# Performance work log

Measured on AMD Instinct MI355X. Metric: run time of the kernel, lower is better.

Reference implementation:

```python
import jax, jax.numpy as jnp
import numpy as np
from jax import lax

DN = ('NCHW', 'OIHW', 'NCHW')

def conv2d(x, w, b, stride, pad):
    y = lax.conv_general_dilated(x, w, (stride, stride), [(pad, pad), (pad, pad)], dimension_numbers=DN)
    return y + b[None, :, None, None]

def conv_transpose2d(x, w, b):
    # torch ConvTranspose2d(k=4, s=2, p=1): weight is (in, out, kH, kW).
    # Equivalent dilated conv: flip spatial dims, swap in/out, lhs_dilation=2, pad=k-1-p=2.
    kernel = jnp.flip(w, (2, 3)).transpose(1, 0, 2, 3)  # (out, in, 4, 4)
    y = lax.conv_general_dilated(x, kernel, (1, 1), [(2, 2), (2, 2)], lhs_dilation=(2, 2), dimension_numbers=DN)
    return y + b[None, :, None, None]

def res_block(x, w, b):
    return x + jax.nn.relu(conv2d(x, w, b, 1, 1))

def setup_inputs() -> dict:
    key = jax.random.key(0)
    ks = jax.random.split(key, 20)
    F_, K, D = 16, 64, 16  # num_features, num_embeddings, embedding_dim
    s = 0.05
    inp = {
        'x': jax.random.normal(ks[0], (64, 1, 256, 256), jnp.float32),
        'conv1_w': jax.random.normal(ks[1], (F_, 1, 4, 4), jnp.float32) * s,
        'conv1_b': jnp.zeros((F_,), jnp.float32),
        'conv2_w': jax.random.normal(ks[2], (F_, F_, 4, 4), jnp.float32) * s,
        'conv2_b': jnp.zeros((F_,), jnp.float32),
        'er1_w': jax.random.normal(ks[3], (F_, F_, 3, 3), jnp.float32) * s,
        'er1_b': jnp.zeros((F_,), jnp.float32),
        'er2_w': jax.random.normal(ks[4], (F_, F_, 3, 3), jnp.float32) * s,
        'er2_b': jnp.zeros((F_,), jnp.float32),
        'codebook': jax.random.normal(ks[5], (K, D), jnp.float32),
        'dr1_w': jax.random.normal(ks[6], (F_, F_, 3, 3), jnp.float32) * s,
        'dr1_b': jnp.zeros((F_,), jnp.float32),
        'dr2_w': jax.random.normal(ks[7], (F_, F_, 3, 3), jnp.float32) * s,
        'dr2_b': jnp.zeros((F_,), jnp.float32),
        'tc1_w': jax.random.normal(ks[8], (F_, F_, 4, 4), jnp.float32) * s,  # ConvTranspose (in,out,kH,kW)
        'tc1_b': jnp.zeros((F_,), jnp.float32),
        'tc2_w': jax.random.normal(ks[9], (F_, 1, 4, 4), jnp.float32) * s,
        'tc2_b': jnp.zeros((1,), jnp.float32),
    }
    return inp

def reference(x, conv1_w, conv1_b, conv2_w, conv2_b, er1_w, er1_b, er2_w, er2_b,
              codebook, dr1_w, dr1_b, dr2_w, dr2_b, tc1_w, tc1_b, tc2_w, tc2_b):
    # Encoder
    h = jax.nn.relu(conv2d(x, conv1_w, conv1_b, 2, 1))
    h = jax.nn.relu(conv2d(h, conv2_w, conv2_b, 2, 1))
    h = res_block(h, er1_w, er1_b)
    h = res_block(h, er2_w, er2_b)  # (B, 16, 64, 64)
    # VQ: faithful to torch's encoded.view(-1, C) raw NCHW flatten
    C = h.shape[1]
    flat = h.reshape(-1, C)  # (N, 16)
    # squared L2 distances without materializing (N, K, D) broadcast tensor
    d = (jnp.sum(flat * flat, axis=1, keepdims=True)
         - 2.0 * flat @ codebook.T
         + jnp.sum(codebook * codebook, axis=1)[None, :])  # (N, K)
    indices = jnp.argmin(d, axis=1)  # (N,)
    quantized = codebook[indices].reshape(h.shape)
    # Decoder
    q = res_block(quantized, dr1_w, dr1_b)
    q = res_block(q, dr2_w, dr2_b)
    q = jax.nn.relu(conv_transpose2d(q, tc1_w, tc1_b))
    decoded = conv_transpose2d(q, tc2_w, tc2_b)  # (B, 1, 256, 256)
    return decoded, indices
```

## Files before the change

kernel.cpp:

```cpp
#include <hip/hip_runtime.h>
#include <hip/hip_bf16.h>


#define R8X(M)  M(0) M(1) M(2) M(3) M(4) M(5) M(6) M(7)

typedef __attribute__((ext_vector_type(8))) short          bf16x8;
typedef __attribute__((ext_vector_type(8))) unsigned short u16x8;
typedef __attribute__((ext_vector_type(4))) float          f32x4;

__device__ __forceinline__ unsigned short f2bf(float f) {
    unsigned u; __builtin_memcpy(&u, &f, 4);
    unsigned r = u + 0x7FFFu + ((u >> 16) & 1u);
    return (unsigned short)(r >> 16);
}
__device__ __forceinline__ float bf2f(unsigned short h) {
    unsigned u = ((unsigned)h) << 16;
    float f; __builtin_memcpy(&f, &u, 4);
    return f;
}

__global__ __launch_bounds__(256) void conv1_k(const float* __restrict__ x, const float* __restrict__ w,
                                               const float* __restrict__ bias,
                                               unsigned short* __restrict__ oh, unsigned short* __restrict__ ol) {
    int idx = blockIdx.x * 256 + threadIdx.x;
    int ox = idx & 127;
    int oy = (idx >> 7) & 127;
    int b  = idx >> 14;
    const float* xin = x + (size_t)b * 65536;
    float pv[16];
#pragma unroll
    for (int ky = 0; ky < 4; ++ky) {
        int iy = 2 * oy - 1 + ky;
#pragma unroll
        for (int kx = 0; kx < 4; ++kx) {
            int ix = 2 * ox - 1 + kx;
            pv[ky * 4 + kx] = (iy >= 0 && iy < 256 && ix >= 0 && ix < 256)
                                  ? xin[iy * 256 + ix] : 0.f;
        }
    }
    u16x8 h0, h1, l0, l1;
#pragma unroll
    for (int oc = 0; oc < 16; ++oc) {
        float acc = bias[oc];
#pragma unroll
        for (int k = 0; k < 16; ++k) acc = fmaf(pv[k], w[oc * 16 + k], acc);
        float r = fmaxf(acc, 0.f);
        unsigned short hb = f2bf(r);
        unsigned short lb = f2bf(r - bf2f(hb));
        if (oc < 8) { h0[oc] = hb; l0[oc] = lb; }
        else        { h1[oc - 8] = hb; l1[oc - 8] = lb; }
    }
    u16x8* po = (u16x8*)(oh + (size_t)idx * 16);
    po[0] = h0; po[1] = h1;
    u16x8* pl = (u16x8*)(ol + (size_t)idx * 16);
    pl[0] = l0; pl[1] = l1;
}

__global__ __launch_bounds__(256) void conv2_mfma_k(const unsigned short* __restrict__ fh,
                                                    const unsigned short* __restrict__ fl,
                                                    const float* __restrict__ w, const float* __restrict__ bias,
                                                    unsigned short* __restrict__ oh, unsigned short* __restrict__ ol) {
    __shared__ unsigned short wsh[16 * 264];
    __shared__ unsigned short wsl[16 * 264];
    for (int i = threadIdx.x; i < 4096; i += 256) {
        int oc = i >> 8, k = i & 255;
        int ic = k & 15, tap = k >> 4;
        float f = w[oc * 256 + ic * 16 + tap];
        unsigned short hb = f2bf(f);
        wsh[oc * 264 + k] = hb;
        wsl[oc * 264 + k] = f2bf(f - bf2f(hb));
    }
    __syncthreads();

    int wid  = threadIdx.x >> 6;
    int lane = threadIdx.x & 63;
    int col = lane & 15;
    int kg  = lane >> 4;
    int ic0 = (kg & 1) * 8;
    float accb = bias[col];
    int gw = blockIdx.x * 4 + wid;

    for (int t = 0; t < 2; ++t) {
        int tile = gw * 2 + t;
        int v0  = (tile & 3) * 16;
        int y   = (tile >> 2) & 63;
        int img = tile >> 8;
        const unsigned short* bh = fh + (size_t)img * 262144;
        const unsigned short* bl = fl + (size_t)img * 262144;
        f32x4 acc = { accb, accb, accb, accb };
#pragma unroll
        for (int m = 0; m < 8; ++m) {
            int tap = 2 * m + (kg >> 1);
            int ty = tap >> 2, tx = tap & 3;
            int jy = 2 * y - 1 + ty;
            int jx = 2 * (v0 + col) - 1 + tx;
            bf16x8 ah = { 0, 0, 0, 0, 0, 0, 0, 0 };
            bf16x8 al = { 0, 0, 0, 0, 0, 0, 0, 0 };
            if (jy >= 0 && jy < 128 && jx >= 0 && jx < 128) {
                size_t off = ((size_t)(jy * 128 + jx)) * 16 + ic0;
                ah = *(const bf16x8*)(bh + off);
                al = *(const bf16x8*)(bl + off);
            }
            bf16x8 wh = *(const bf16x8*)&wsh[col * 264 + m * 32 + kg * 8];
            bf16x8 wl = *(const bf16x8*)&wsl[col * 264 + m * 32 + kg * 8];
            acc = __builtin_amdgcn_mfma_f32_16x16x32_bf16(ah, wh, acc, 0, 0, 0);
            acc = __builtin_amdgcn_mfma_f32_16x16x32_bf16(al, wh, acc, 0, 0, 0);
            acc = __builtin_amdgcn_mfma_f32_16x16x32_bf16(ah, wl, acc, 0, 0, 0);
        }
#pragma unroll
        for (int r = 0; r < 4; ++r) {
            int xx = v0 + kg * 4 + r;
            size_t ad = (size_t)img * 65536 + ((size_t)(y * 64 + xx)) * 16 + col;
            float rv = fmaxf(acc[r], 0.f);
            unsigned short hb = f2bf(rv);
            oh[ad] = hb;
            ol[ad] = f2bf(rv - bf2f(hb));
        }
    }
}

template <int OUTMODE>
__global__ __launch_bounds__(256) void er_mfma_k(const unsigned short* __restrict__ inh,
                                                 const unsigned short* __restrict__ inl,
                                                 const float* __restrict__ w, const float* __restrict__ bias,
                                                 unsigned short* __restrict__ oh, unsigned short* __restrict__ ol,
                                                 float* __restrict__ ofp) {
    __shared__ unsigned short wsh[16 * 176];
    __shared__ unsigned short wsl[16 * 176];
    for (int i = threadIdx.x; i < 2816; i += 256) {
        int oc = i / 176, k = i % 176;
        float f = (k < 144) ? w[(oc * 16 + (k & 15)) * 9 + (k >> 4)] : 0.f;
        unsigned short hb = f2bf(f);
        wsh[i] = hb;
        wsl[i] = f2bf(f - bf2f(hb));
    }
    __syncthreads();

    int wid  = threadIdx.x >> 6;
    int lane = threadIdx.x & 63;
    int col = lane & 15;
    int kg  = lane >> 4;
    int ic0 = (kg & 1) * 8;
    float accb = bias[col];
    int gw = blockIdx.x * 4 + wid;

    for (int t = 0; t < 8; ++t) {
        int tile = gw * 8 + t;
        int v0  = (tile & 3) * 16;
        int y   = (tile >> 2) & 63;
        int img = tile >> 8;
        const unsigned short* xh = inh + (size_t)img * 65536;
        const unsigned short* xl = inl + (size_t)img * 65536;
        f32x4 acc = { accb, accb, accb, accb };
#pragma unroll
        for (int m = 0; m < 5; ++m) {
            int tap = 2 * m + (kg >> 1);
            bf16x8 ah = { 0, 0, 0, 0, 0, 0, 0, 0 };
            bf16x8 al = { 0, 0, 0, 0, 0, 0, 0, 0 };
            if (tap < 9) {
                int ty = tap / 3, tx = tap - ty * 3;
                int jy = y + ty - 1;
                int jx = v0 + col + tx - 1;
                if (jy >= 0 && jy < 64 && jx >= 0 && jx < 64) {
                    size_t off = ((size_t)(jy * 64 + jx)) * 16 + ic0;
                    ah = *(const bf16x8*)(xh + off);
                    al = *(const bf16x8*)(xl + off);
                }
            }
            bf16x8 wh = *(const bf16x8*)&wsh[col * 176 + m * 32 + kg * 8];
            bf16x8 wl = *(const bf16x8*)&wsl[col * 176 + m * 32 + kg * 8];
            acc = __builtin_amdgcn_mfma_f32_16x16x32_bf16(ah, wh, acc, 0, 0, 0);
            acc = __builtin_amdgcn_mfma_f32_16x16x32_bf16(al, wh, acc, 0, 0, 0);
            acc = __builtin_amdgcn_mfma_f32_16x16x32_bf16(ah, wl, acc, 0, 0, 0);
        }
#pragma unroll
        for (int r = 0; r < 4; ++r) {
            int px = v0 + kg * 4 + r;
            size_t ad = ((size_t)(y * 64 + px)) * 16 + col;
            float vin = bf2f(xh[ad]) + bf2f(xl[ad]);
            float res = vin + fmaxf(acc[r], 0.f);
            if (OUTMODE == 0) {
                unsigned short hb = f2bf(res);
                oh[(size_t)img * 65536 + ad] = hb;
                ol[(size_t)img * 65536 + ad] = f2bf(res - bf2f(hb));
            } else {
                ofp[(size_t)img * 65536 + (size_t)col * 4096 + y * 64 + px] = res;
            }
        }
    }
}

__global__ __launch_bounds__(256) void vq_k(const float* __restrict__ h, const float* __restrict__ cb,
                                            unsigned short* __restrict__ q, float* __restrict__ idx_out) {
    __shared__ float cbs[1024];
    __shared__ float cn[64];
    for (int i = threadIdx.x; i < 1024; i += 256) cbs[i] = cb[i];
    __syncthreads();
    if (threadIdx.x < 64) {
        float s = 0.f;
#pragma unroll
        for (int d = 0; d < 16; ++d) { float v = cbs[threadIdx.x * 16 + d]; s = fmaf(v, v, s); }
        cn[threadIdx.x] = s;
    }
    __syncthreads();
    int r = blockIdx.x * 256 + threadIdx.x;
    float f[16];
    const float4* hp = (const float4*)(h + (size_t)r * 16);
#pragma unroll
    for (int j = 0; j < 4; ++j) {
        float4 v = hp[j];
        f[j * 4 + 0] = v.x; f[j * 4 + 1] = v.y; f[j * 4 + 2] = v.z; f[j * 4 + 3] = v.w;
    }
    float best = 3.4e38f;
    int bi = 0;
    for (int k = 0; k < 64; ++k) {
        float dot = 0.f;
#pragma unroll
        for (int d = 0; d < 16; ++d) dot = fmaf(f[d], cbs[k * 16 + d], dot);
        float dist = cn[k] - 2.f * dot;
        if (dist < best) { best = dist; bi = k; }
    }
    u16x8 q0, q1;
#pragma unroll
    for (int d = 0; d < 8; ++d) {
        q0[d] = f2bf(cbs[bi * 16 + d]);
        q1[d] = f2bf(cbs[bi * 16 + 8 + d]);
    }
    u16x8* qp = (u16x8*)(q + (size_t)r * 16);
    qp[0] = q0; qp[1] = q1;
    idx_out[r] = (float)bi;
}

__global__ __launch_bounds__(256) void trans_k(const unsigned short* __restrict__ in,
                                               unsigned short* __restrict__ out) {
    __shared__ unsigned short lds[16 * 64];
    int b = blockIdx.x >> 6;
    int y = blockIdx.x & 63;
    int t = threadIdx.x;
    {
        int c = t >> 4, x0 = (t & 15) * 4;
        const unsigned short* p = in + (((size_t)(b * 16 + c) * 64 + y) << 6) + x0;
#pragma unroll
        for (int j = 0; j < 4; ++j) lds[c * 64 + x0 + j] = p[j];
    }
    __syncthreads();
    {
        int xx = t >> 2, c0 = (t & 3) * 4;
        unsigned short* p = out + (((size_t)(b * 64 + y) * 64 + xx) << 4) + c0;
#pragma unroll
        for (int j = 0; j < 4; ++j) p[j] = lds[(c0 + j) * 64 + xx];
    }
}

__global__ __launch_bounds__(256) void res_mfma_k(const unsigned short* __restrict__ in,
                                                  const float* __restrict__ w, const float* __restrict__ bias,
                                                  unsigned short* __restrict__ outb) {
    int wid  = threadIdx.x >> 6;
    int lane = threadIdx.x & 63;
    int col = lane & 15;
    int kg  = lane >> 4;
    int ic0 = (kg & 1) * 8;

    bf16x8 bw[5];
#pragma unroll
    for (int m = 0; m < 5; ++m) {
        int tap = 2 * m + (kg >> 1);
        bf16x8 t = { 0, 0, 0, 0, 0, 0, 0, 0 };
        if (tap < 9) {
#pragma unroll
            for (int j = 0; j < 8; ++j)
                t[j] = (short)f2bf(w[(col * 16 + ic0 + j) * 9 + tap]);
        }
        bw[m] = t;
    }
    float accb = bias[col];

    int gw = blockIdx.x * 4 + wid;
    for (int t = 0; t < 8; ++t) {
        int tile = gw * 8 + t;
        int v0  = (tile & 3) * 16;
        int y   = (tile >> 2) & 63;
        int img = tile >> 8;
        const unsigned short* xi = in + (size_t)img * 65536;
        f32x4 acc = { accb, accb, accb, accb };
#pragma unroll
        for (int m = 0; m < 5; ++m) {
            int tap = 2 * m + (kg >> 1);
            bf16x8 a = { 0, 0, 0, 0, 0, 0, 0, 0 };
            if (tap < 9) {
                int ty = tap / 3, tx = tap - ty * 3;
                int jy = y + ty - 1;
                int jx = v0 + col + tx - 1;
                if (jy >= 0 && jy < 64 && jx >= 0 && jx < 64)
                    a = *(const bf16x8*)(xi + ((jy * 64 + jx) * 16 + ic0));
            }
            acc = __builtin_amdgcn_mfma_f32_16x16x32_bf16(a, bw[m], acc, 0, 0, 0);
        }
#pragma unroll
        for (int r = 0; r < 4; ++r) {
            int px = v0 + kg * 4 + r;
            size_t ad = (size_t)(y * 64 + px) * 16 + col;
            float vin = bf2f(xi[ad]);
            outb[(size_t)img * 65536 + ad] = f2bf(vin + fmaxf(acc[r], 0.f));
        }
    }
}

__global__ __launch_bounds__(256) void tconv1_mfma_k(const unsigned short* __restrict__ xb,
                                                     const float* __restrict__ w1, const float* __restrict__ bia,
                                                     unsigned short* __restrict__ outb) {
    int cls = blockIdx.x >> 9;
    int bb  = blockIdx.x & 511;
    int DY = cls >> 1, DX = cls & 1;
    int wid  = threadIdx.x >> 6;
    int lane = threadIdx.x & 63;
    int oc = lane & 15;
    int kg = lane >> 4;

    bf16x8 bfr0, bfr1;
    float accb = bia[oc];
#pragma unroll
    for (int m = 0; m < 2; ++m) {
        int tap = 2 * m + (kg >> 1);
        int ty = tap >> 1, tx = tap & 1;
        int koff = (3 - DY - 2 * ty) * 4 + (3 - DX - 2 * tx);
        int ic0 = (kg & 1) * 8;
        bf16x8 t;
#pragma unroll
        for (int j = 0; j < 8; ++j)
            t[j] = (short)f2bf(w1[(ic0 + j) * 256 + oc * 16 + koff]);
        if (m == 0) bfr0 = t; else bfr1 = t;
    }

    int Wc = bb * 4 + wid;
    for (int t = 0; t < 8; ++t) {
        int tile = Wc * 8 + t;
        int v0  = (tile & 3) * 16;
        int u   = (tile >> 2) & 63;
        int img = tile >> 8;
        const unsigned short* xi = xb + (size_t)img * 65536;
        f32x4 acc = { accb, accb, accb, accb };
#pragma unroll
        for (int m = 0; m < 2; ++m) {
            int tap = 2 * m + (kg >> 1);
            int ty = tap >> 1, tx = tap & 1;
            int jy = u + DY - 1 + ty;
            int jx = v0 + oc + DX - 1 + tx;
            bf16x8 a = { 0, 0, 0, 0, 0, 0, 0, 0 };
            if (jy >= 0 && jy < 64 && jx >= 0 && jx < 64) {
                int ic0 = (kg & 1) * 8;
                a = *(const bf16x8*)(xi + ((jy * 64 + jx) * 16 + ic0));
            }
            acc = __builtin_amdgcn_mfma_f32_16x16x32_bf16(a, (m == 0 ? bfr0 : bfr1), acc, 0, 0, 0);
        }
        int my = 2 * u + DY;
#pragma unroll
        for (int r = 0; r < 4; ++r) {
            int pxr = kg * 4 + r;
            int mx  = 2 * (v0 + pxr) + DX;
            outb[(((size_t)img * 16384) + my * 128 + mx) * 16 + oc] = f2bf(fmaxf(acc[r], 0.f));
        }
    }
}

template <int RY, int RX>
__device__ __forceinline__ void quad_contrib(const unsigned short* __restrict__ px,
                                             const float* __restrict__ w2,
                                             float& a00, float& a01, float& a10, float& a11) {
    constexpr int nY = (RY == 0) ? 2 : 1;
    constexpr int nX = (RX == 0) ? 2 : 1;
    constexpr int dyA[2] = { (RY == 1) ? 1 : 0, 1 };
    constexpr int kyA[2] = { (RY == -1) ? 3 : ((RY == 0) ? 1 : 0), 2 };
    constexpr int dxA[2] = { (RX == 1) ? 1 : 0, 1 };
    constexpr int kxA[2] = { (RX == -1) ? 3 : ((RX == 0) ? 1 : 0), 2 };
    u16x8 h0 = *(const u16x8*)px;
    u16x8 h1 = *(const u16x8*)(px + 8);
#pragma unroll
    for (int iy = 0; iy < nY; ++iy) {
#pragma unroll
        for (int ix = 0; ix < nX; ++ix) {
            const int ky = kyA[iy], kx = kxA[ix];
            float& a = (dyA[iy] == 0) ? ((dxA[ix] == 0) ? a00 : a01)
                                      : ((dxA[ix] == 0) ? a10 : a11);
#pragma unroll
            for (int ic = 0; ic < 8; ++ic)
                a = fmaf(bf2f(h0[ic]), w2[ic * 16 + ky * 4 + kx], a);
#pragma unroll
            for (int ic = 0; ic < 8; ++ic)
                a = fmaf(bf2f(h1[ic]), w2[(ic + 8) * 16 + ky * 4 + kx], a);
        }
    }
}

__global__ __launch_bounds__(256) void tconv2_quad_k(const unsigned short* __restrict__ f1b,
                                                     const float* __restrict__ w2, const float* __restrict__ b2,
                                                     float* __restrict__ out) {
    int idx = blockIdx.x * 256 + threadIdx.x;
    int v = idx & 127;
    int u = (idx >> 7) & 127;
    int b = idx >> 14;
    const unsigned short* fb = f1b + (size_t)b * 262144;
    float b2s = b2[0];
    float a00 = b2s, a01 = b2s, a10 = b2s, a11 = b2s;

#define QC(RY, RX) { int jy = u + (RY), jx = v + (RX); \
    if (jy >= 0 && jy < 128 && jx >= 0 && jx < 128) \
        quad_contrib<RY, RX>(fb + ((size_t)(jy * 128 + jx) << 4), w2, a00, a01, a10, a11); }
    QC(-1, -1) QC(-1, 0) QC(-1, 1)
    QC( 0, -1) QC( 0, 0) QC( 0, 1)
    QC( 1, -1) QC( 1, 0) QC( 1, 1)
#undef QC

    float* o = out + (size_t)b * 65536 + (2 * u) * 256 + 2 * v;
    float2 r0; r0.x = a00; r0.y = a01;
    float2 r1; r1.x = a10; r1.y = a11;
    *(float2*)o         = r0;
    *(float2*)(o + 256) = r1;
}

extern "C" void kernel_launch(void* const* d_in, const int* in_sizes, int n_in,
                              void* d_out, int out_size, void* d_ws, size_t ws_size,
                              hipStream_t stream) {
    const float* x    = (const float*)d_in[0];
    const float* c1w  = (const float*)d_in[1];
    const float* c1b  = (const float*)d_in[2];
    const float* c2w  = (const float*)d_in[3];
    const float* c2b  = (const float*)d_in[4];
    const float* er1w = (const float*)d_in[5];
    const float* er1b = (const float*)d_in[6];
    const float* er2w = (const float*)d_in[7];
    const float* er2b = (const float*)d_in[8];
    const float* cb   = (const float*)d_in[9];
    const float* dr1w = (const float*)d_in[10];
    const float* dr1b = (const float*)d_in[11];
    const float* dr2w = (const float*)d_in[12];
    const float* dr2b = (const float*)d_in[13];
    const float* t1w  = (const float*)d_in[14];
    const float* t1b  = (const float*)d_in[15];
    const float* t2w  = (const float*)d_in[16];
    const float* t2b  = (const float*)d_in[17];

    char* W = (char*)d_ws;
    const size_t MB = 1024 * 1024;
    unsigned short* f1h = (unsigned short*)(W + 0);
    unsigned short* f1l = (unsigned short*)(W + 32 * MB);
    unsigned short* c2h = (unsigned short*)(W + 64 * MB);
    unsigned short* c2l = (unsigned short*)(W + 80 * MB);
    unsigned short* e1h = (unsigned short*)(W + 96 * MB);
    unsigned short* e1l = (unsigned short*)(W + 112 * MB);
    float*          e2f = (float*)         (W + 128 * MB);
    unsigned short* qn  = (unsigned short*)(W + 152 * MB);
    unsigned short* qc  = (unsigned short*)(W + 168 * MB);
    unsigned short* d1o = (unsigned short*)(W + 184 * MB);
    unsigned short* d2o = (unsigned short*)(W + 200 * MB);
    unsigned short* t1o = (unsigned short*)(W + 216 * MB);

    float* out     = (float*)d_out;
    float* idx_out = out + 4194304;

    conv1_k      <<<4096, 256, 0, stream>>>(x, c1w, c1b, f1h, f1l);
    conv2_mfma_k <<<2048, 256, 0, stream>>>(f1h, f1l, c2w, c2b, c2h, c2l);
    er_mfma_k<0> <<< 512, 256, 0, stream>>>(c2h, c2l, er1w, er1b, e1h, e1l, nullptr);
    er_mfma_k<1> <<< 512, 256, 0, stream>>>(e1h, e1l, er2w, er2b, nullptr, nullptr, e2f);
    vq_k         <<<1024, 256, 0, stream>>>(e2f, cb, qn, idx_out);
    trans_k      <<<4096, 256, 0, stream>>>(qn, qc);
    res_mfma_k   <<< 512, 256, 0, stream>>>(qc, dr1w, dr1b, d1o);
    res_mfma_k   <<< 512, 256, 0, stream>>>(d1o, dr2w, dr2b, d2o);
    tconv1_mfma_k<<<2048, 256, 0, stream>>>(d2o, t1w, t1b, t1o);
    tconv2_quad_k<<<4096, 256, 0, stream>>>(t1o, t2w, t2b, out);
}
```

Before: 214.1 us.

## Fuse VQ output transpose into vq kernel and double grid for res convs

```diff
diff --git a/kernel.cpp b/kernel.cpp
--- a/kernel.cpp
+++ b/kernel.cpp
@@ -144,8 +144,8 @@
     float accb = bias[col];
     int gw = blockIdx.x * 4 + wid;
 
-    for (int t = 0; t < 8; ++t) {
-        int tile = gw * 8 + t;
+    for (int t = 0; t < 4; ++t) {
+        int tile = gw * 4 + t;
         int v0  = (tile & 3) * 16;
         int y   = (tile >> 2) & 63;
         int img = tile >> 8;
@@ -191,9 +191,10 @@
 }
 
 __global__ __launch_bounds__(256) void vq_k(const float* __restrict__ h, const float* __restrict__ cb,
-                                            unsigned short* __restrict__ q, float* __restrict__ idx_out) {
+                                            unsigned short* __restrict__ qc, float* __restrict__ idx_out) {
     __shared__ float cbs[1024];
     __shared__ float cn[64];
+    __shared__ unsigned short st[4096];
     for (int i = threadIdx.x; i < 1024; i += 256) cbs[i] = cb[i];
     __syncthreads();
     if (threadIdx.x < 64) {
@@ -203,7 +204,16 @@
         cn[threadIdx.x] = s;
     }
     __syncthreads();
-    int r = blockIdx.x * 256 + threadIdx.x;
+
+    int blk = blockIdx.x;
+    int b  = blk >> 4;
+    int y0 = (blk & 15) * 4;
+    int t  = threadIdx.x;
+    int c  = t >> 4;
+    int yl = (t >> 2) & 3;
+    int xc = t & 3;
+    int r  = b * 4096 + c * 256 + (y0 + yl) * 4 + xc;
+
     float f[16];
     const float4* hp = (const float4*)(h + (size_t)r * 16);
 #pragma unroll
@@ -220,36 +230,18 @@
         float dist = cn[k] - 2.f * dot;
         if (dist < best) { best = dist; bi = k; }
     }
-    u16x8 q0, q1;
-#pragma unroll
-    for (int d = 0; d < 8; ++d) {
-        q0[d] = f2bf(cbs[bi * 16 + d]);
-        q1[d] = f2bf(cbs[bi * 16 + 8 + d]);
-    }
-    u16x8* qp = (u16x8*)(q + (size_t)r * 16);
-    qp[0] = q0; qp[1] = q1;
     idx_out[r] = (float)bi;
-}
-
-__global__ __launch_bounds__(256) void trans_k(const unsigned short* __restrict__ in,
-                                               unsigned short* __restrict__ out) {
-    __shared__ unsigned short lds[16 * 64];
-    int b = blockIdx.x >> 6;
-    int y = blockIdx.x & 63;
-    int t = threadIdx.x;
-    {
-        int c = t >> 4, x0 = (t & 15) * 4;
-        const unsigned short* p = in + (((size_t)(b * 16 + c) * 64 + y) << 6) + x0;
-#pragma unroll
-        for (int j = 0; j < 4; ++j) lds[c * 64 + x0 + j] = p[j];
-    }
+
+#pragma unroll
+    for (int j = 0; j < 16; ++j)
+        st[((yl * 64) + (xc * 16 + j)) * 16 + c] = f2bf(cbs[bi * 16 + j]);
     __syncthreads();
-    {
-        int xx = t >> 2, c0 = (t & 3) * 4;
-        unsigned short* p = out + (((size_t)(b * 64 + y) * 64 + xx) << 4) + c0;
-#pragma unroll
-        for (int j = 0; j < 4; ++j) p[j] = lds[(c0 + j) * 64 + xx];
-    }
+
+    u16x8* dst = (u16x8*)(qc + (((size_t)(b * 64 + y0)) * 64) * 16);
+    const u16x8* src = (const u16x8*)st;
+#pragma unroll
+    for (int i = 0; i < 2; ++i)
+        dst[t + 256 * i] = src[t + 256 * i];
 }
 
 __global__ __launch_bounds__(256) void res_mfma_k(const unsigned short* __restrict__ in,
@@ -276,8 +268,8 @@
     float accb = bias[col];
 
     int gw = blockIdx.x * 4 + wid;
-    for (int t = 0; t < 8; ++t) {
-        int tile = gw * 8 + t;
+    for (int t = 0; t < 4; ++t) {
+        int tile = gw * 4 + t;
         int v0  = (tile & 3) * 16;
         int y   = (tile >> 2) & 63;
         int img = tile >> 8;
@@ -449,23 +441,21 @@
     unsigned short* e1h = (unsigned short*)(W + 96 * MB);
     unsigned short* e1l = (unsigned short*)(W + 112 * MB);
     float*          e2f = (float*)         (W + 128 * MB);
-    unsigned short* qn  = (unsigned short*)(W + 152 * MB);
-    unsigned short* qc  = (unsigned short*)(W + 168 * MB);
-    unsigned short* d1o = (unsigned short*)(W + 184 * MB);
-    unsigned short* d2o = (unsigned short*)(W + 200 * MB);
-    unsigned short* t1o = (unsigned short*)(W + 216 * MB);
+    unsigned short* qc  = (unsigned short*)(W + 152 * MB);
+    unsigned short* d1o = (unsigned short*)(W + 168 * MB);
+    unsigned short* d2o = (unsigned short*)(W + 184 * MB);
+    unsigned short* t1o = (unsigned short*)(W + 200 * MB);
 
     float* out     = (float*)d_out;
     float* idx_out = out + 4194304;
 
     conv1_k      <<<4096, 256, 0, stream>>>(x, c1w, c1b, f1h, f1l);
     conv2_mfma_k <<<2048, 256, 0, stream>>>(f1h, f1l, c2w, c2b, c2h, c2l);
-    er_mfma_k<0> <<< 512, 256, 0, stream>>>(c2h, c2l, er1w, er1b, e1h, e1l, nullptr);
-    er_mfma_k<1> <<< 512, 256, 0, stream>>>(e1h, e1l, er2w, er2b, nullptr, nullptr, e2f);
-    vq_k         <<<1024, 256, 0, stream>>>(e2f, cb, qn, idx_out);
-    trans_k      <<<4096, 256, 0, stream>>>(qn, qc);
-    res_mfma_k   <<< 512, 256, 0, stream>>>(qc, dr1w, dr1b, d1o);
-    res_mfma_k   <<< 512, 256, 0, stream>>>(d1o, dr2w, dr2b, d2o);
+    er_mfma_k<0> <<<1024, 256, 0, stream>>>(c2h, c2l, er1w, er1b, e1h, e1l, nullptr);
+    er_mfma_k<1> <<<1024, 256, 0, stream>>>(e1h, e1l, er2w, er2b, nullptr, nullptr, e2f);
+    vq_k         <<<1024, 256, 0, stream>>>(e2f, cb, qc, idx_out);
+    res_mfma_k   <<<1024, 256, 0, stream>>>(qc, dr1w, dr1b, d1o);
+    res_mfma_k   <<<1024, 256, 0, stream>>>(d1o, dr2w, dr2b, d2o);
     tconv1_mfma_k<<<2048, 256, 0, stream>>>(d2o, t1w, t1b, t1o);
     tconv2_quad_k<<<4096, 256, 0, stream>>>(t1o, t2w, t2b, out);
 }
```

New measurement: 202.7 us. -5.3%, faster.
